# Performance work log

Measured on AMD Instinct MI355X. Metric: run time of the kernel, lower is better.

The kernel has to match this reference:

```python
import jax, jax.numpy as jnp
import numpy as np

DIM = 768
NUM_HEADS = 12
HEAD_DIM = DIM // NUM_HEADS
B, V, L = 1, 8, 512


def _block_mask_bias(V, L, dtype):
    # allowed[v_q, v_k]: views 0,1 attend to views 0,1 (incl. self); views >=2 causal (v_q >= v_k)
    vq = jnp.arange(V)[:, None]
    vk = jnp.arange(V)[None, :]
    allowed = ((vq <= 1) & (vk <= 1)) | (vq >= vk)  # [V, V]
    allowed = jnp.repeat(jnp.repeat(allowed, L, axis=0), L, axis=1)  # [V*L, V*L]
    neg_inf = jnp.asarray(-jnp.inf, dtype)
    return jnp.where(allowed, jnp.asarray(0.0, dtype), neg_inf)


def setup_inputs() -> dict:
    key = jax.random.key(0)
    k0, k1, k2, k3, k4, k5 = jax.random.split(key, 6)
    s = 1.0 / np.sqrt(DIM)
    x = jax.random.normal(k0, (B, V, L, DIM), dtype=jnp.float32)
    Wq = jax.random.normal(k1, (DIM, DIM), dtype=jnp.float32) * s
    Wk = jax.random.normal(k2, (DIM, DIM), dtype=jnp.float32) * s
    Wv = jax.random.normal(k3, (DIM, DIM), dtype=jnp.float32) * s
    Wo = jax.random.normal(k4, (DIM, DIM), dtype=jnp.float32) * s
    bo = jax.random.normal(k5, (DIM,), dtype=jnp.float32) * 0.01
    return {"x": x, "Wq": Wq, "Wk": Wk, "Wv": Wv, "Wo": Wo, "bo": bo}


def reference(x, Wq, Wk, Wv, Wo, bo):
    Bx, Vx, Lx, C = x.shape
    S = Vx * Lx
    H, D = NUM_HEADS, HEAD_DIM
    scale = D ** -0.5

    xf = x.reshape(Bx, S, C)
    # linear projections (no bias, qkv_bias=False), split heads -> [B, H, S, D]
    def split_heads(t):
        return t.reshape(Bx, S, H, D).transpose(0, 2, 1, 3)
    q = split_heads(xf @ Wq.T)
    k = split_heads(xf @ Wk.T)
    v = split_heads(xf @ Wv.T)

    bias = _block_mask_bias(Vx, Lx, q.dtype)  # [S, S], broadcast over B, H
    scores = jnp.einsum("bhqd,bhkd->bhqk", q, k) * scale + bias
    attn = jax.nn.softmax(scores, axis=-1)
    out = jnp.einsum("bhqk,bhkd->bhqd", attn, v)  # [B, H, S, D]
    out = out.transpose(0, 2, 1, 3).reshape(Bx, Vx, Lx, C)
    return out @ Wo.T + bo
```

## Files before the change

kernel.cpp:

```cpp
#include <hip/hip_runtime.h>

#define S_TOT 4096
#define C_DIM 768
#define QKV_LD 2304
#define NH 12
#define QSCALE 0.18033688011112042f

using f32x4  = __attribute__((ext_vector_type(4))) float;
using bf16x8 = __attribute__((ext_vector_type(8))) __bf16;

#if __has_builtin(__builtin_amdgcn_exp2f)
#define EXP2(x) __builtin_amdgcn_exp2f(x)
#else
#define EXP2(x) exp2f(x)
#endif

#define DRAIN_AND_BARRIER()                                     \
  do {                                                          \
    asm volatile("s_waitcnt vmcnt(0) lgkmcnt(0)" ::: "memory"); \
    __builtin_amdgcn_sched_barrier(0);                          \
    __syncthreads();                                            \
  } while (0)

__device__ inline unsigned short f2bf_bits(float f) {
  unsigned int u = __float_as_uint(f);
  u = (u + 0x7FFFu + ((u >> 16) & 1u)) >> 16;
  return (unsigned short)u;
}
__device__ inline __bf16 f2bf(float f) {
  unsigned short s = f2bf_bits(f);
  __bf16 b;
  __builtin_memcpy(&b, &s, 2);
  return b;
}

__device__ __forceinline__ void gl_lds16(const __bf16* g, __bf16* l) {
  __builtin_amdgcn_global_load_lds(
      (__attribute__((address_space(1))) void*)(g),
      (__attribute__((address_space(3))) void*)(l), 16, 0, 0);
}

__global__ void cvt_all(const float* __restrict__ x, const float* __restrict__ Wq,
                        const float* __restrict__ Wk, const float* __restrict__ Wv,
                        const float* __restrict__ Wo, __bf16* __restrict__ dst) {
  const int XN = S_TOT * C_DIM;
  const int WN = C_DIM * C_DIM;
  int i = (blockIdx.x * blockDim.x + threadIdx.x) * 4;
  if (i >= XN + 4 * WN) return;
  const float* src; float scale = 1.f; int off;
  if (i < XN)               { src = x;  off = i; }
  else if (i < XN + WN)     { src = Wq; off = i - XN; scale = QSCALE; }
  else if (i < XN + 2 * WN) { src = Wk; off = i - XN - WN; }
  else if (i < XN + 3 * WN) { src = Wv; off = i - XN - 2 * WN; }
  else                      { src = Wo; off = i - XN - 3 * WN; }
  float4 v = *reinterpret_cast<const float4*>(src + off);
  ushort4 o;
  o.x = f2bf_bits(v.x * scale); o.y = f2bf_bits(v.y * scale);
  o.z = f2bf_bits(v.z * scale); o.w = f2bf_bits(v.w * scale);
  *reinterpret_cast<ushort4*>(reinterpret_cast<unsigned short*>(dst) + i) = o;
}

template<bool OUT_BIAS_F32, bool SPLIT_V>
__global__ __launch_bounds__(256) void gemm128(
    const __bf16* __restrict__ A, const __bf16* __restrict__ B,
    void* __restrict__ Cv, const float* __restrict__ bias,
    __bf16* __restrict__ VtOut, int K, int ldc) {
  __shared__ __bf16 As[128][64];
  __shared__ __bf16 Bs[128][64];
  const int t = threadIdx.x, lane = t & 63, wv = t >> 6;
  const int wr = wv >> 1, wc = wv & 1;
  const int lhi = lane >> 4, llo = lane & 15;
  const int m0 = blockIdx.y * 128, n0 = blockIdx.x * 128;

  f32x4 acc[4][4];
  #pragma unroll
  for (int a = 0; a < 4; ++a)
    #pragma unroll
    for (int b = 0; b < 4; ++b) acc[a][b] = (f32x4){0.f, 0.f, 0.f, 0.f};

  for (int kt = 0; kt < K; kt += 64) {
    __syncthreads();
    #pragma unroll
    for (int n = 0; n < 4; ++n) {
      const int ci = n * 256 + wv * 64 + lane;
      const int r = ci >> 3;
      const int cc = (ci & 7) ^ (r & 7);
      gl_lds16(A + (size_t)(m0 + r) * K + kt + cc * 8, &As[0][0] + ci * 8);
      gl_lds16(B + (size_t)(n0 + r) * K + kt + cc * 8, &Bs[0][0] + ci * 8);
    }
    DRAIN_AND_BARRIER();
    #pragma unroll
    for (int kk = 0; kk < 2; ++kk) {
      bf16x8 af[4], bfr[4];
      #pragma unroll
      for (int mi = 0; mi < 4; ++mi) {
        const int row = wr * 64 + mi * 16 + llo;
        af[mi] = *reinterpret_cast<const bf16x8*>(
            &As[0][0] + row * 64 + (((kk << 2) | lhi) ^ (llo & 7)) * 8);
      }
      #pragma unroll
      for (int ni = 0; ni < 4; ++ni) {
        const int row = wc * 64 + ni * 16 + llo;
        bfr[ni] = *reinterpret_cast<const bf16x8*>(
            &Bs[0][0] + row * 64 + (((kk << 2) | lhi) ^ (llo & 7)) * 8);
      }
      #pragma unroll
      for (int mi = 0; mi < 4; ++mi)
        #pragma unroll
        for (int ni = 0; ni < 4; ++ni)
          acc[mi][ni] = __builtin_amdgcn_mfma_f32_16x16x32_bf16(af[mi], bfr[ni], acc[mi][ni], 0, 0, 0);
    }
  }

  if (SPLIT_V && n0 >= 1536) {
    const int head = (n0 - 1536 + wc * 64) >> 6;
    const int tile64 = (m0 >> 6) + wr;
    #pragma unroll
    for (int mi = 0; mi < 4; ++mi) {
      const int p = (mi >> 1) * 32 + lhi * 8 + (mi & 1) * 4;
      #pragma unroll
      for (int ni = 0; ni < 4; ++ni) {
        const int d = ni * 16 + llo;
        ushort4 o;
        o.x = f2bf_bits(acc[mi][ni][0]); o.y = f2bf_bits(acc[mi][ni][1]);
        o.z = f2bf_bits(acc[mi][ni][2]); o.w = f2bf_bits(acc[mi][ni][3]);
        uint2 u; __builtin_memcpy(&u, &o, 8);
        *reinterpret_cast<uint2*>(VtOut + ((size_t)head * 64 + d) * S_TOT + tile64 * 64 + p) = u;
      }
    }
    return;
  }

  #pragma unroll
  for (int mi = 0; mi < 4; ++mi)
    #pragma unroll
    for (int ni = 0; ni < 4; ++ni)
      #pragma unroll
      for (int i = 0; i < 4; ++i) {
        const int row = m0 + wr * 64 + mi * 16 + lhi * 4 + i;
        const int col = n0 + wc * 64 + ni * 16 + llo;
        if constexpr (OUT_BIAS_F32) {
          reinterpret_cast<float*>(Cv)[(size_t)row * ldc + col] = acc[mi][ni][i] + bias[col];
        } else {
          reinterpret_cast<__bf16*>(Cv)[(size_t)row * ldc + col] = f2bf(acc[mi][ni][i]);
        }
      }
}

__global__ __launch_bounds__(256) void attn_fused7(
    const __bf16* __restrict__ QKV, const __bf16* __restrict__ Vtp,
    __bf16* __restrict__ att) {
  __shared__ __bf16 Ks[3][64][64];
  __shared__ __bf16 Vs[3][64][64];
  const int t = threadIdx.x, lane = t & 63, wv = t >> 6;
  const int llo = lane & 15, hi = lane >> 4;
  const int sw = llo & 7;
  const int j = blockIdx.x;
  const int s = j & 255, r3 = j >> 8;
  const int p = (r3 == 0) ? s : (r3 == 1 ? 511 - s : 512 + s);
  const int pq = p / 12;
  const int qb = 63 - pq;
  const int h = p - pq * 12;
  const int q0 = qb * 64;
  const int vq = q0 >> 9;
  const int kv_end = (vq <= 1) ? 1024 : (vq + 1) * 512;
  const int n_tiles = kv_end >> 6;
  const int myq = q0 + wv * 16 + llo;

  bf16x8 qf[2];
  {
    const __bf16* qrow = QKV + (size_t)myq * QKV_LD + h * 64;
    qf[0] = *reinterpret_cast<const bf16x8*>(qrow + hi * 8);
    qf[1] = *reinterpret_cast<const bf16x8*>(qrow + 32 + hi * 8);
  }
  asm volatile("s_waitcnt vmcnt(0)" ::: "memory");

  f32x4 Oa[4];
  #pragma unroll
  for (int dt = 0; dt < 4; ++dt) Oa[dt] = (f32x4){0.f, 0.f, 0.f, 0.f};
  float l = 0.f;

  auto stage = [&](int k0, int buf) {
    #pragma unroll
    for (int n = 0; n < 2; ++n) {
      const int ci = (wv * 2 + n) * 64 + lane;
      const int r = ci >> 3;
      const int cc = (ci & 7) ^ (r & 7);
      gl_lds16(QKV + (size_t)(k0 + r) * QKV_LD + C_DIM + h * 64 + cc * 8,
               &Ks[buf][0][0] + (wv * 2 + n) * 512);
      gl_lds16(Vtp + ((size_t)h * 64 + r) * S_TOT + k0 + cc * 8,
               &Vs[buf][0][0] + (wv * 2 + n) * 512);
    }
  };

  stage(0, 0);
  stage(64, 1);
  int cur = 0;
  for (int tt = 0; tt < n_tiles; ++tt) {
    if (tt + 1 < n_tiles) {
      asm volatile("s_waitcnt vmcnt(4)" ::: "memory");
    } else {
      asm volatile("s_waitcnt vmcnt(0)" ::: "memory");
    }
    __builtin_amdgcn_sched_barrier(0);
    __builtin_amdgcn_s_barrier();
    __builtin_amdgcn_sched_barrier(0);
    if (tt + 2 < n_tiles) {
      const int nxt = (cur + 2 >= 3) ? cur - 1 : cur + 2;
      stage((tt + 2) * 64, nxt);
    }
    const __bf16* Kb = &Ks[cur][0][0];
    const __bf16* Vb = &Vs[cur][0][0];

    f32x4 sc[4];
    #pragma unroll
    for (int nt = 0; nt < 4; ++nt) sc[nt] = (f32x4){0.f, 0.f, 0.f, 0.f};
    #pragma unroll
    for (int nt = 0; nt < 4; ++nt) {
      const __bf16* kr = Kb + (nt * 16 + llo) * 64;
      bf16x8 kf0 = *reinterpret_cast<const bf16x8*>(kr + ((hi ^ sw) * 8));
      bf16x8 kf1 = *reinterpret_cast<const bf16x8*>(kr + (((4 + hi) ^ sw) * 8));
      sc[nt] = __builtin_amdgcn_mfma_f32_16x16x32_bf16(kf0, qf[0], sc[nt], 0, 0, 0);
      sc[nt] = __builtin_amdgcn_mfma_f32_16x16x32_bf16(kf1, qf[1], sc[nt], 0, 0, 0);
    }

    float pp[4][4];
    #pragma unroll
    for (int nt = 0; nt < 4; ++nt)
      #pragma unroll
      for (int i = 0; i < 4; ++i) pp[nt][i] = EXP2(sc[nt][i]);
    float t0 = (pp[0][0] + pp[0][1]) + (pp[0][2] + pp[0][3]);
    float t1 = (pp[1][0] + pp[1][1]) + (pp[1][2] + pp[1][3]);
    float t2 = (pp[2][0] + pp[2][1]) + (pp[2][2] + pp[2][3]);
    float t3 = (pp[3][0] + pp[3][1]) + (pp[3][2] + pp[3][3]);
    l += (t0 + t1) + (t2 + t3);

    bf16x8 pf[2];
    #pragma unroll
    for (int mm = 0; mm < 2; ++mm)
      #pragma unroll
      for (int jj = 0; jj < 8; ++jj)
        pf[mm][jj] = (__bf16)pp[2 * mm + (jj >> 2)][jj & 3];

    #pragma unroll
    for (int dt = 0; dt < 4; ++dt) {
      const __bf16* vr = Vb + (dt * 16 + llo) * 64;
      #pragma unroll
      for (int mm = 0; mm < 2; ++mm) {
        bf16x8 va = *reinterpret_cast<const bf16x8*>(vr + (((mm * 4 + hi) ^ sw) * 8));
        Oa[dt] = __builtin_amdgcn_mfma_f32_16x16x32_bf16(va, pf[mm], Oa[dt], 0, 0, 0);
      }
    }
    cur = (cur + 1 == 3) ? 0 : cur + 1;
  }

  l += __shfl_xor(l, 16);
  l += __shfl_xor(l, 32);
  const float inv = 1.f / l;
  #pragma unroll
  for (int dt = 0; dt < 4; ++dt) {
    ushort4 o;
    o.x = f2bf_bits(Oa[dt][0] * inv);
    o.y = f2bf_bits(Oa[dt][1] * inv);
    o.z = f2bf_bits(Oa[dt][2] * inv);
    o.w = f2bf_bits(Oa[dt][3] * inv);
    *reinterpret_cast<ushort4*>(att + (size_t)myq * C_DIM + h * 64 + dt * 16 + hi * 4) = o;
  }
}

extern "C" void kernel_launch(void* const* d_in, const int* in_sizes, int n_in,
                              void* d_out, int out_size, void* d_ws, size_t ws_size,
                              hipStream_t stream) {
  const float* x  = (const float*)d_in[0];
  const float* Wq = (const float*)d_in[1];
  const float* Wk = (const float*)d_in[2];
  const float* Wv = (const float*)d_in[3];
  const float* Wo = (const float*)d_in[4];
  const float* bo = (const float*)d_in[5];

  __bf16* xb   = (__bf16*)d_ws;
  __bf16* Wqkv = xb + (size_t)S_TOT * C_DIM;
  __bf16* Wob  = Wqkv + (size_t)3 * C_DIM * C_DIM;
  __bf16* QKV  = Wob + (size_t)C_DIM * C_DIM;
  __bf16* Vtp  = QKV + (size_t)S_TOT * QKV_LD;
  __bf16* att  = Vtp + (size_t)NH * 64 * S_TOT;

  {
    const int tot = S_TOT * C_DIM + 4 * C_DIM * C_DIM;
    cvt_all<<<dim3((tot / 4 + 255) / 256), dim3(256), 0, stream>>>(
        x, Wq, Wk, Wv, Wo, xb);
  }

  gemm128<false, true><<<dim3(QKV_LD / 128, S_TOT / 128), dim3(256), 0, stream>>>(
      xb, Wqkv, (void*)QKV, nullptr, Vtp, C_DIM, QKV_LD);

  attn_fused7<<<dim3(768), dim3(256), 0, stream>>>(QKV, Vtp, att);

  gemm128<true, false><<<dim3(C_DIM / 128, S_TOT / 128), dim3(256), 0, stream>>>(
      att, Wob, d_out, bo, nullptr, C_DIM, C_DIM);
}
```

Measured before the change: 106.1 us.

## Double attention query tile to 128 rows with 8 waves and custom block schedule

The attention kernel now processes 128 query rows per block with 512 threads (8 waves), halving the grid to 384 blocks so each staged K/V tile in shared memory is reused by twice as many queries. A hand-written decode table maps block indices to (query block, head) pairs to balance the causal workload across the grid. Staging is simplified so each thread issues one K and one V async load per tile using incrementing pointers. The trade-off is fewer blocks for load balancing and higher per-block register and thread pressure.

```diff
diff --git a/kernel.cpp b/kernel.cpp
--- a/kernel.cpp
+++ b/kernel.cpp
@@ -147,7 +147,27 @@
       }
 }
 
-__global__ __launch_bounds__(256) void attn_fused7(
+__device__ __forceinline__ void decode_qh(int j, int& qb, int& h) {
+  if (j >= 256) {
+    const int i = j - 256;
+    if (i < 16)       { qb = (i & 3);            h = 4 + (i >> 2); }
+    else if (i < 64)  { const int k = i - 16;  qb = 4 + (k & 3);  h = k >> 2; }
+    else if (i < 112) { const int k = i - 64;  qb = 8 + (k & 3);  h = k >> 2; }
+    else              { const int k = i - 112; qb = (k & 3);      h = 8 + (k >> 2); }
+  } else if (j >= 128) {
+    const int i = j - 128;
+    if (i < 48)       { qb = 28 + (i & 3);     h = i >> 2; }
+    else if (i < 96)  { const int k = i - 48;  qb = 24 + (k & 3); h = k >> 2; }
+    else              { const int k = i - 96;  qb = 20 + (k & 3); h = k >> 2; }
+  } else {
+    if (j < 16)       { qb = 20 + (j & 3);     h = 8 + (j >> 2); }
+    else if (j < 64)  { const int k = j - 16;  qb = 16 + (k & 3); h = k >> 2; }
+    else if (j < 112) { const int k = j - 64;  qb = 12 + (k & 3); h = k >> 2; }
+    else              { const int k = j - 112; qb = (k & 3);      h = k >> 2; }
+  }
+}
+
+__global__ __launch_bounds__(512) void attn_fused8(
     const __bf16* __restrict__ QKV, const __bf16* __restrict__ Vtp,
     __bf16* __restrict__ att) {
   __shared__ __bf16 Ks[3][64][64];
@@ -155,14 +175,10 @@
   const int t = threadIdx.x, lane = t & 63, wv = t >> 6;
   const int llo = lane & 15, hi = lane >> 4;
   const int sw = llo & 7;
-  const int j = blockIdx.x;
-  const int s = j & 255, r3 = j >> 8;
-  const int p = (r3 == 0) ? s : (r3 == 1 ? 511 - s : 512 + s);
-  const int pq = p / 12;
-  const int qb = 63 - pq;
-  const int h = p - pq * 12;
-  const int q0 = qb * 64;
-  const int vq = q0 >> 9;
+  int qb, h;
+  decode_qh((int)blockIdx.x, qb, h);
+  const int q0 = qb * 128;
+  const int vq = qb >> 2;
   const int kv_end = (vq <= 1) ? 1024 : (vq + 1) * 512;
   const int n_tiles = kv_end >> 6;
   const int myq = q0 + wv * 16 + llo;
@@ -180,25 +196,26 @@
   for (int dt = 0; dt < 4; ++dt) Oa[dt] = (f32x4){0.f, 0.f, 0.f, 0.f};
   float l = 0.f;
 
-  auto stage = [&](int k0, int buf) {
-    #pragma unroll
-    for (int n = 0; n < 2; ++n) {
-      const int ci = (wv * 2 + n) * 64 + lane;
-      const int r = ci >> 3;
-      const int cc = (ci & 7) ^ (r & 7);
-      gl_lds16(QKV + (size_t)(k0 + r) * QKV_LD + C_DIM + h * 64 + cc * 8,
-               &Ks[buf][0][0] + (wv * 2 + n) * 512);
-      gl_lds16(Vtp + ((size_t)h * 64 + r) * S_TOT + k0 + cc * 8,
-               &Vs[buf][0][0] + (wv * 2 + n) * 512);
-    }
+  const int r = t >> 3;
+  const int cc = (t & 7) ^ (r & 7);
+  const __bf16* kp = QKV + (size_t)r * QKV_LD + C_DIM + h * 64 + cc * 8;
+  const __bf16* vp = Vtp + ((size_t)h * 64 + r) * S_TOT + cc * 8;
+  __bf16* const kdst = &Ks[0][0][0] + (size_t)wv * 512;
+  __bf16* const vdst = &Vs[0][0][0] + (size_t)wv * 512;
+
+  auto stage = [&](int buf) {
+    gl_lds16(kp, kdst + (size_t)buf * 4096);
+    gl_lds16(vp, vdst + (size_t)buf * 4096);
+    kp += (size_t)64 * QKV_LD;
+    vp += 64;
   };
 
-  stage(0, 0);
-  stage(64, 1);
+  stage(0);
+  stage(1);
   int cur = 0;
   for (int tt = 0; tt < n_tiles; ++tt) {
     if (tt + 1 < n_tiles) {
-      asm volatile("s_waitcnt vmcnt(4)" ::: "memory");
+      asm volatile("s_waitcnt vmcnt(2)" ::: "memory");
     } else {
       asm volatile("s_waitcnt vmcnt(0)" ::: "memory");
     }
@@ -207,7 +224,7 @@
     __builtin_amdgcn_sched_barrier(0);
     if (tt + 2 < n_tiles) {
       const int nxt = (cur + 2 >= 3) ? cur - 1 : cur + 2;
-      stage((tt + 2) * 64, nxt);
+      stage(nxt);
     }
     const __bf16* Kb = &Ks[cur][0][0];
     const __bf16* Vb = &Vs[cur][0][0];
@@ -294,7 +311,7 @@
   gemm128<false, true><<<dim3(QKV_LD / 128, S_TOT / 128), dim3(256), 0, stream>>>(
       xb, Wqkv, (void*)QKV, nullptr, Vtp, C_DIM, QKV_LD);
 
-  attn_fused7<<<dim3(768), dim3(256), 0, stream>>>(QKV, Vtp, att);
+  attn_fused8<<<dim3(384), dim3(512), 0, stream>>>(QKV, Vtp, att);
 
   gemm128<true, false><<<dim3(C_DIM / 128, S_TOT / 128), dim3(256), 0, stream>>>(
       att, Wob, d_out, bo, nullptr, C_DIM, C_DIM);
```

New measurement: 109.5 us. 1.03x slower.

## Split long causal query blocks across two KV halves and merge partials

Applied to the files above, without the earlier changes.

Query blocks in views 4-7, which have the longest KV ranges, are now processed by two workgroups, each covering half of the KV range. Each half writes an unnormalized fp32 output and row sum to workspace, and a new merge kernel combines and normalizes them. The grid grows from 768 to 1152 blocks in a hand-ordered schedule meant to balance per-block work and cut the tail from long blocks. The staging code also now uses precomputed, incrementing pointers. The cost is an extra kernel launch plus fp32 partial traffic. The merge is only valid if no running-max subtraction is applied, which the unshown softmax code appears to assume.

```diff
diff --git a/kernel.cpp b/kernel.cpp
--- a/kernel.cpp
+++ b/kernel.cpp
@@ -147,24 +147,32 @@
       }
 }
 
-__global__ __launch_bounds__(256) void attn_fused7(
+__device__ __forceinline__ void decode9(int j, int& qb64, int& h, int& half, bool& split) {
+  if (j < 192)      { split = true;  half = j & 1;  qb64 = 56 + ((j >> 1) & 7); h = j >> 4; }
+  else if (j < 288) { int k = j - 192; split = false; half = 0; qb64 = 24 + (k & 7); h = k >> 3; }
+  else if (j < 480) { int k = j - 288; split = true;  half = k & 1; qb64 = 48 + ((k >> 1) & 7); h = k >> 4; }
+  else if (j < 672) { int k = j - 480; split = true;  half = k & 1; qb64 = 40 + ((k >> 1) & 7); h = k >> 4; }
+  else if (j < 768) { int k = j - 672; split = false; half = 0; qb64 = 16 + (k & 7); h = k >> 3; }
+  else if (j < 960) { int k = j - 768; split = true;  half = k & 1; qb64 = 32 + ((k >> 1) & 7); h = k >> 4; }
+  else              { int k = j - 960; split = false; half = 0; qb64 = k & 15; h = k >> 4; }
+}
+
+__global__ __launch_bounds__(256) void attn_fused9(
     const __bf16* __restrict__ QKV, const __bf16* __restrict__ Vtp,
-    __bf16* __restrict__ att) {
+    __bf16* __restrict__ att, float* __restrict__ Opart,
+    float* __restrict__ lpart) {
   __shared__ __bf16 Ks[3][64][64];
   __shared__ __bf16 Vs[3][64][64];
   const int t = threadIdx.x, lane = t & 63, wv = t >> 6;
   const int llo = lane & 15, hi = lane >> 4;
   const int sw = llo & 7;
-  const int j = blockIdx.x;
-  const int s = j & 255, r3 = j >> 8;
-  const int p = (r3 == 0) ? s : (r3 == 1 ? 511 - s : 512 + s);
-  const int pq = p / 12;
-  const int qb = 63 - pq;
-  const int h = p - pq * 12;
-  const int q0 = qb * 64;
-  const int vq = q0 >> 9;
+  int qb64, h, half; bool split;
+  decode9((int)blockIdx.x, qb64, h, half, split);
+  const int vq = qb64 >> 3;
   const int kv_end = (vq <= 1) ? 1024 : (vq + 1) * 512;
-  const int n_tiles = kv_end >> 6;
+  const int n_tiles = split ? (kv_end >> 7) : (kv_end >> 6);
+  const int kstart = split ? half * (kv_end >> 1) : 0;
+  const int q0 = qb64 * 64;
   const int myq = q0 + wv * 16 + llo;
 
   bf16x8 qf[2];
@@ -180,21 +188,29 @@
   for (int dt = 0; dt < 4; ++dt) Oa[dt] = (f32x4){0.f, 0.f, 0.f, 0.f};
   float l = 0.f;
 
-  auto stage = [&](int k0, int buf) {
-    #pragma unroll
-    for (int n = 0; n < 2; ++n) {
-      const int ci = (wv * 2 + n) * 64 + lane;
-      const int r = ci >> 3;
-      const int cc = (ci & 7) ^ (r & 7);
-      gl_lds16(QKV + (size_t)(k0 + r) * QKV_LD + C_DIM + h * 64 + cc * 8,
-               &Ks[buf][0][0] + (wv * 2 + n) * 512);
-      gl_lds16(Vtp + ((size_t)h * 64 + r) * S_TOT + k0 + cc * 8,
-               &Vs[buf][0][0] + (wv * 2 + n) * 512);
-    }
+  const int ci0 = (wv * 2 + 0) * 64 + lane, r0 = ci0 >> 3, c0 = (ci0 & 7) ^ (r0 & 7);
+  const int ci1 = (wv * 2 + 1) * 64 + lane, r1 = ci1 >> 3, c1 = (ci1 & 7) ^ (r1 & 7);
+  const __bf16* kp0 = QKV + (size_t)(kstart + r0) * QKV_LD + C_DIM + h * 64 + c0 * 8;
+  const __bf16* kp1 = QKV + (size_t)(kstart + r1) * QKV_LD + C_DIM + h * 64 + c1 * 8;
+  const __bf16* vp0 = Vtp + ((size_t)h * 64 + r0) * S_TOT + kstart + c0 * 8;
+  const __bf16* vp1 = Vtp + ((size_t)h * 64 + r1) * S_TOT + kstart + c1 * 8;
+  __bf16* const kd0 = &Ks[0][0][0] + ci0 * 8 - lane * 8;
+  __bf16* const kd1 = &Ks[0][0][0] + ci1 * 8 - lane * 8;
+  __bf16* const vd0 = &Vs[0][0][0] + ci0 * 8 - lane * 8;
+  __bf16* const vd1 = &Vs[0][0][0] + ci1 * 8 - lane * 8;
+
+  auto stage = [&](int buf) {
+    const size_t bo = (size_t)buf * 4096;
+    gl_lds16(kp0, kd0 + bo);
+    gl_lds16(vp0, vd0 + bo);
+    gl_lds16(kp1, kd1 + bo);
+    gl_lds16(vp1, vd1 + bo);
+    kp0 += (size_t)64 * QKV_LD; kp1 += (size_t)64 * QKV_LD;
+    vp0 += 64; vp1 += 64;
   };
 
-  stage(0, 0);
-  stage(64, 1);
+  stage(0);
+  stage(1);
   int cur = 0;
   for (int tt = 0; tt < n_tiles; ++tt) {
     if (tt + 1 < n_tiles) {
@@ -207,7 +223,7 @@
     __builtin_amdgcn_sched_barrier(0);
     if (tt + 2 < n_tiles) {
       const int nxt = (cur + 2 >= 3) ? cur - 1 : cur + 2;
-      stage((tt + 2) * 64, nxt);
+      stage(nxt);
     }
     const __bf16* Kb = &Ks[cur][0][0];
     const __bf16* Vb = &Vs[cur][0][0];
@@ -256,15 +272,49 @@
 
   l += __shfl_xor(l, 16);
   l += __shfl_xor(l, 32);
-  const float inv = 1.f / l;
+  if (!split) {
+    const float inv = 1.f / l;
+    #pragma unroll
+    for (int dt = 0; dt < 4; ++dt) {
+      ushort4 o;
+      o.x = f2bf_bits(Oa[dt][0] * inv);
+      o.y = f2bf_bits(Oa[dt][1] * inv);
+      o.z = f2bf_bits(Oa[dt][2] * inv);
+      o.w = f2bf_bits(Oa[dt][3] * inv);
+      *reinterpret_cast<ushort4*>(att + (size_t)myq * C_DIM + h * 64 + dt * 16 + hi * 4) = o;
+    }
+  } else {
+    const int slot = ((qb64 - 32) * 12 + h) * 2 + half;
+    float* Ob = Opart + (((size_t)slot * 64) + wv * 16 + llo) * 64;
+    #pragma unroll
+    for (int dt = 0; dt < 4; ++dt)
+      *reinterpret_cast<f32x4*>(Ob + dt * 16 + hi * 4) = Oa[dt];
+    if (hi == 0) lpart[slot * 64 + wv * 16 + llo] = l;
+  }
+}
+
+__global__ __launch_bounds__(256) void merge9(
+    const float* __restrict__ Opart, const float* __restrict__ lpart,
+    __bf16* __restrict__ att) {
+  const int b = blockIdx.x;
+  const int qi = b / 12, h = b - qi * 12;
+  const int t = threadIdx.x;
+  const int r = t >> 2, d0 = (t & 3) * 16;
+  const int slot0 = b * 2;
+  const float* O0 = Opart + ((size_t)slot0 * 64 + r) * 64 + d0;
+  const float* O1 = Opart + ((size_t)(slot0 + 1) * 64 + r) * 64 + d0;
+  const float linv = 1.f / (lpart[slot0 * 64 + r] + lpart[(slot0 + 1) * 64 + r]);
+  __bf16* dst = att + ((size_t)(qi + 32) * 64 + r) * C_DIM + h * 64 + d0;
   #pragma unroll
-  for (int dt = 0; dt < 4; ++dt) {
+  for (int i = 0; i < 4; ++i) {
+    f32x4 a = *reinterpret_cast<const f32x4*>(O0 + i * 4);
+    f32x4 c = *reinterpret_cast<const f32x4*>(O1 + i * 4);
     ushort4 o;
-    o.x = f2bf_bits(Oa[dt][0] * inv);
-    o.y = f2bf_bits(Oa[dt][1] * inv);
-    o.z = f2bf_bits(Oa[dt][2] * inv);
-    o.w = f2bf_bits(Oa[dt][3] * inv);
-    *reinterpret_cast<ushort4*>(att + (size_t)myq * C_DIM + h * 64 + dt * 16 + hi * 4) = o;
+    o.x = f2bf_bits((a[0] + c[0]) * linv);
+    o.y = f2bf_bits((a[1] + c[1]) * linv);
+    o.z = f2bf_bits((a[2] + c[2]) * linv);
+    o.w = f2bf_bits((a[3] + c[3]) * linv);
+    *reinterpret_cast<ushort4*>(dst + i * 4) = o;
   }
 }
 
@@ -284,6 +334,8 @@
   __bf16* QKV  = Wob + (size_t)C_DIM * C_DIM;
   __bf16* Vtp  = QKV + (size_t)S_TOT * QKV_LD;
   __bf16* att  = Vtp + (size_t)NH * 64 * S_TOT;
+  float*  Opart = (float*)(att + (size_t)S_TOT * C_DIM);
+  float*  lpart = Opart + (size_t)768 * 64 * 64;
 
   {
     const int tot = S_TOT * C_DIM + 4 * C_DIM * C_DIM;
@@ -294,7 +346,9 @@
   gemm128<false, true><<<dim3(QKV_LD / 128, S_TOT / 128), dim3(256), 0, stream>>>(
       xb, Wqkv, (void*)QKV, nullptr, Vtp, C_DIM, QKV_LD);
 
-  attn_fused7<<<dim3(768), dim3(256), 0, stream>>>(QKV, Vtp, att);
+  attn_fused9<<<dim3(1152), dim3(256), 0, stream>>>(QKV, Vtp, att, Opart, lpart);
+
+  merge9<<<dim3(384), dim3(256), 0, stream>>>(Opart, lpart, att);
 
   gemm128<true, false><<<dim3(C_DIM / 128, S_TOT / 128), dim3(256), 0, stream>>>(
       att, Wob, d_out, bo, nullptr, C_DIM, C_DIM);
```

After: 101.2 us. 4.6% less time.
